# Kernel tuning notes

Hardware: AMD Instinct MI355X
Metric: run time of the kernel (lower is better)

The kernel has to match this reference:

```python
import jax, jax.numpy as jnp
import numpy as np

B, N, K, T = 64, 32768, 128, 512
TMAX = 512  # number of discrete time bins (round(t*10) range)


def setup_inputs() -> dict:
    key = jax.random.key(0)
    k1, k2, k3, k4, k5, k6 = jax.random.split(key, 6)
    state = jax.random.normal(k1, (B, N, 4), dtype=jnp.float32)
    time_idx = jax.random.randint(k2, (B, N), 0, TMAX, dtype=jnp.int32)
    # unique_ids in [-1, K-1]; -1 marks clutter (invalid) measurements
    unique_ids = jax.random.randint(k3, (B, N), 0, K + 1, dtype=jnp.int32) - 1
    # trajectory states [B,K,T,5]: cols [x, y, vx, vy, t] with round(t*10) in 0..TMAX-1
    xy = jax.random.normal(k4, (B, K, T, 2), dtype=jnp.float32)
    vel = jax.random.normal(k5, (B, K, T, 2), dtype=jnp.float32)
    # per-(b,k) permutation of 0..T-1 -> unique times within each trajectory
    times = jnp.argsort(jax.random.uniform(k6, (B, K, T)), axis=-1).astype(jnp.float32)
    traj_states = jnp.concatenate([xy, vel, (times / 10.0)[..., None]], axis=-1)
    return {"state": state, "time_idx": time_idx, "unique_ids": unique_ids,
            "traj_states": traj_states}


def reference(state, time_idx, unique_ids, traj_states):
    xy = state[..., :2]                                   # [B,N,2]
    tvals = jnp.round(traj_states[..., 4] * 10.0).astype(jnp.int32)  # [B,K,T]
    traj_xy = traj_states[..., :2]                        # [B,K,T,2]
    # dense lookup table [B,K,TMAX,2]; default 0 matches torch.zeros_like(tgt)
    b_ix = jnp.arange(B)[:, None, None]
    k_ix = jnp.arange(K)[None, :, None]
    table = jnp.zeros((B, K, TMAX, 2), dtype=state.dtype)
    table = table.at[b_ix, k_ix, tvals].set(traj_xy, mode="drop")
    # gather tgt per measurement by (object id, time bin)
    obj = jnp.clip(unique_ids, 0, K - 1)
    tcl = jnp.clip(time_idx, 0, TMAX - 1)
    tgt = table[jnp.arange(B)[:, None], obj, tcl]         # [B,N,2]
    valid = unique_ids >= 0
    tgt = jnp.where(valid[..., None], tgt, 0.0)
    diff = jnp.abs(xy - tgt).sum(-1)                      # [B,N]
    vf = valid.astype(state.dtype)
    loss = (diff * vf).sum() / vf.sum()
    return loss
```

## Files before the change

kernel.cpp:

```cpp
#include <hip/hip_runtime.h>
#include <hip/hip_fp16.h>

constexpr int Bc = 64;
constexpr int Nc = 32768;
constexpr int Kc = 128;
constexpr int Tc = 512;
constexpr int TMAXc = 512;
constexpr int BK = Bc * Kc;

typedef float f32x4 __attribute__((ext_vector_type(4)));

constexpr size_t TABLE_BYTES = (size_t)Bc * Kc * TMAXc * 4;
constexpr int NBLK2 = 1024;

__global__ __launch_bounds__(256) void build_table_k(
    const f32x4* __restrict__ traj4,
    uint2* __restrict__ table2)
{
    __shared__ __align__(16) float    stage[Tc * 5];
    __shared__ __align__(8)  unsigned tbl[TMAXc];

    const int j   = blockIdx.x;
    const int xcd = j & 7;
    const int s   = j >> 3;
    const int b   = ((s >> 7) << 3) | xcd;
    const int k   = s & 127;
    const int bk  = (b << 7) | k;

    const f32x4* src = traj4 + (size_t)bk * 640;
    for (int t = threadIdx.x; t < 640; t += 256) {
        ((f32x4*)stage)[t] = __builtin_nontemporal_load(&src[t]);
    }
    __syncthreads();

    #pragma unroll
    for (int r = 0; r < 2; ++r) {
        int t = threadIdx.x + r * 256;
        float x  = stage[t * 5 + 0];
        float y  = stage[t * 5 + 1];
        float tv = stage[t * 5 + 4];
        int tau = __float2int_rn(tv * 10.0f);
        if ((unsigned)tau < (unsigned)TMAXc) {
            __half2 p = __floats2half2_rn(x, y);
            unsigned raw;
            __builtin_memcpy(&raw, &p, 4);
            tbl[tau] = raw;
        }
    }
    __syncthreads();

    table2[(size_t)bk * 256 + threadIdx.x] = ((const uint2*)tbl)[threadIdx.x];
}

__global__ __launch_bounds__(256) void gather_reduce_k(
    const f32x4*    __restrict__ state,
    const int*      __restrict__ tidx,
    const int*      __restrict__ uid,
    const unsigned* __restrict__ table,
    float2*         __restrict__ partials)
{
    const int j     = blockIdx.x;
    const int xcd   = j & 7;
    const int s     = j >> 3;
    const int b     = ((s >> 4) << 3) | xcd;
    const int chunk = s & 15;
    const int base  = (b << 15) + (chunk << 11);
    const unsigned* tb = table + ((long long)b << 16);

    f32x4    sv[8];
    int      idv[8], tiv[8];
    unsigned tg[8];

    #pragma unroll
    for (int r = 0; r < 8; ++r) {
        int i = base + r * 256 + threadIdx.x;
        sv[r]  = __builtin_nontemporal_load(&state[i]);
        idv[r] = __builtin_nontemporal_load(&uid[i]);
        tiv[r] = __builtin_nontemporal_load(&tidx[i]);
    }
    #pragma unroll
    for (int r = 0; r < 8; ++r) {
        int obj = min(max(idv[r], 0), Kc - 1);
        int tcl = min(max(tiv[r], 0), TMAXc - 1);
        tg[r] = tb[(obj << 9) + tcl];
    }
    float sum = 0.0f, cnt = 0.0f;
    #pragma unroll
    for (int r = 0; r < 8; ++r) {
        __half2 p;
        __builtin_memcpy(&p, &tg[r], 4);
        float tx = __low2float(p);
        float ty = __high2float(p);
        if (idv[r] >= 0) {
            sum += fabsf(sv[r].x - tx) + fabsf(sv[r].y - ty);
            cnt += 1.0f;
        }
    }

    #pragma unroll
    for (int off = 32; off > 0; off >>= 1) {
        sum += __shfl_down(sum, off, 64);
        cnt += __shfl_down(cnt, off, 64);
    }
    __shared__ float2 lds[4];
    int lane = threadIdx.x & 63;
    int w    = threadIdx.x >> 6;
    if (lane == 0) lds[w] = make_float2(sum, cnt);
    __syncthreads();
    if (threadIdx.x == 0) {
        float s2 = 0.0f, c2 = 0.0f;
        #pragma unroll
        for (int q = 0; q < 4; ++q) { s2 += lds[q].x; c2 += lds[q].y; }
        partials[j] = make_float2(s2, c2);
    }
}

__global__ __launch_bounds__(1024) void final_reduce_k(
    const float2* __restrict__ partials, float* __restrict__ out)
{
    float s, c;
    {
        float2 p = partials[threadIdx.x];
        s = p.x; c = p.y;
    }
    #pragma unroll
    for (int off = 32; off > 0; off >>= 1) {
        s += __shfl_down(s, off, 64);
        c += __shfl_down(c, off, 64);
    }
    __shared__ float2 lds[16];
    int lane = threadIdx.x & 63;
    int w    = threadIdx.x >> 6;
    if (lane == 0) lds[w] = make_float2(s, c);
    __syncthreads();
    if (threadIdx.x == 0) {
        float s2 = 0.0f, c2 = 0.0f;
        #pragma unroll
        for (int q = 0; q < 16; ++q) { s2 += lds[q].x; c2 += lds[q].y; }
        out[0] = s2 / c2;
    }
}

extern "C" void kernel_launch(void* const* d_in, const int* in_sizes, int n_in,
                              void* d_out, int out_size, void* d_ws, size_t ws_size,
                              hipStream_t stream) {
    const f32x4* state = (const f32x4*)d_in[0];
    const int*   tidx  = (const int*)  d_in[1];
    const int*   uid   = (const int*)  d_in[2];
    const f32x4* traj4 = (const f32x4*)d_in[3];
    float* out = (float*)d_out;

    unsigned* table    = (unsigned*)d_ws;
    float2*   partials = (float2*)((char*)d_ws + TABLE_BYTES);

    build_table_k  <<<BK, 256, 0, stream>>>(traj4, (uint2*)table);
    gather_reduce_k<<<NBLK2, 256, 0, stream>>>(state, tidx, uid, table, partials);
    final_reduce_k <<<1, 1024, 0, stream>>>(partials, out);
}
```

Measured before the change: 40.14 us.

## Process two trajectories per block, halve gather blocks, load only xy state

The table-build kernel now handles two (b,k) trajectories per block, with fully unrolled staging loads and two table rows written per block. The gather kernel loads only the x,y half of each state row as an 8-byte vector instead of the full 16-byte row, and each block handles twice as many measurements with half as many blocks. The final reduce shrinks to match. The goal is to cut state read traffic and per-block launch and sync overhead, at the cost of more registers and fewer blocks in flight to hide gather latency.

After: 38.91 us. 1.03x faster.

```diff
diff --git a/kernel.cpp b/kernel.cpp
--- a/kernel.cpp
+++ b/kernel.cpp
@@ -9,32 +9,36 @@
 constexpr int BK = Bc * Kc;
 
 typedef float f32x4 __attribute__((ext_vector_type(4)));
+typedef float f32x2 __attribute__((ext_vector_type(2)));
 
 constexpr size_t TABLE_BYTES = (size_t)Bc * Kc * TMAXc * 4;
-constexpr int NBLK2 = 1024;
+constexpr int NBLK1 = BK / 2;
+constexpr int NBLK2 = 512;
 
 __global__ __launch_bounds__(256) void build_table_k(
     const f32x4* __restrict__ traj4,
     uint2* __restrict__ table2)
 {
-    __shared__ __align__(16) float    stage[Tc * 5];
-    __shared__ __align__(8)  unsigned tbl[TMAXc];
+    __shared__ __align__(16) float    stage[2 * Tc * 5];
+    __shared__ __align__(8)  unsigned tbl[2 * TMAXc];
 
     const int j   = blockIdx.x;
     const int xcd = j & 7;
     const int s   = j >> 3;
-    const int b   = ((s >> 7) << 3) | xcd;
-    const int k   = s & 127;
-    const int bk  = (b << 7) | k;
+    const int b   = ((s >> 6) << 3) | xcd;
+    const int k2  = s & 63;
+    const int bk0 = (b << 7) | (k2 << 1);
 
-    const f32x4* src = traj4 + (size_t)bk * 640;
-    for (int t = threadIdx.x; t < 640; t += 256) {
+    const f32x4* src = traj4 + (size_t)bk0 * 640;
+    #pragma unroll
+    for (int r = 0; r < 5; ++r) {
+        int t = threadIdx.x + r * 256;
         ((f32x4*)stage)[t] = __builtin_nontemporal_load(&src[t]);
     }
     __syncthreads();
 
     #pragma unroll
-    for (int r = 0; r < 2; ++r) {
+    for (int r = 0; r < 4; ++r) {
         int t = threadIdx.x + r * 256;
         float x  = stage[t * 5 + 0];
         float y  = stage[t * 5 + 1];
@@ -44,16 +48,21 @@
             __half2 p = __floats2half2_rn(x, y);
             unsigned raw;
             __builtin_memcpy(&raw, &p, 4);
-            tbl[tau] = raw;
+            tbl[((t >> 9) << 9) + tau] = raw;
         }
     }
     __syncthreads();
 
-    table2[(size_t)bk * 256 + threadIdx.x] = ((const uint2*)tbl)[threadIdx.x];
+    uint2* dst = table2 + (size_t)bk0 * 256;
+    #pragma unroll
+    for (int r = 0; r < 2; ++r) {
+        int t = threadIdx.x + r * 256;
+        dst[t] = ((const uint2*)tbl)[t];
+    }
 }
 
 __global__ __launch_bounds__(256) void gather_reduce_k(
-    const f32x4*    __restrict__ state,
+    const f32x2*    __restrict__ state2,
     const int*      __restrict__ tidx,
     const int*      __restrict__ uid,
     const unsigned* __restrict__ table,
@@ -62,31 +71,31 @@
     const int j     = blockIdx.x;
     const int xcd   = j & 7;
     const int s     = j >> 3;
-    const int b     = ((s >> 4) << 3) | xcd;
-    const int chunk = s & 15;
-    const int base  = (b << 15) + (chunk << 11);
+    const int b     = ((s >> 3) << 3) | xcd;
+    const int chunk = s & 7;
+    const int base  = (b << 15) + (chunk << 12);
     const unsigned* tb = table + ((long long)b << 16);
 
-    f32x4    sv[8];
-    int      idv[8], tiv[8];
-    unsigned tg[8];
+    f32x2    sv[16];
+    int      idv[16], tiv[16];
+    unsigned tg[16];
 
     #pragma unroll
-    for (int r = 0; r < 8; ++r) {
+    for (int r = 0; r < 16; ++r) {
         int i = base + r * 256 + threadIdx.x;
-        sv[r]  = __builtin_nontemporal_load(&state[i]);
+        sv[r]  = __builtin_nontemporal_load(&state2[2 * (size_t)i]);
         idv[r] = __builtin_nontemporal_load(&uid[i]);
         tiv[r] = __builtin_nontemporal_load(&tidx[i]);
     }
     #pragma unroll
-    for (int r = 0; r < 8; ++r) {
+    for (int r = 0; r < 16; ++r) {
         int obj = min(max(idv[r], 0), Kc - 1);
         int tcl = min(max(tiv[r], 0), TMAXc - 1);
         tg[r] = tb[(obj << 9) + tcl];
     }
     float sum = 0.0f, cnt = 0.0f;
     #pragma unroll
-    for (int r = 0; r < 8; ++r) {
+    for (int r = 0; r < 16; ++r) {
         __half2 p;
         __builtin_memcpy(&p, &tg[r], 4);
         float tx = __low2float(p);
@@ -115,7 +124,7 @@
     }
 }
 
-__global__ __launch_bounds__(1024) void final_reduce_k(
+__global__ __launch_bounds__(512) void final_reduce_k(
     const float2* __restrict__ partials, float* __restrict__ out)
 {
     float s, c;
@@ -128,7 +137,7 @@
         s += __shfl_down(s, off, 64);
         c += __shfl_down(c, off, 64);
     }
-    __shared__ float2 lds[16];
+    __shared__ float2 lds[8];
     int lane = threadIdx.x & 63;
     int w    = threadIdx.x >> 6;
     if (lane == 0) lds[w] = make_float2(s, c);
@@ -136,7 +145,7 @@
     if (threadIdx.x == 0) {
         float s2 = 0.0f, c2 = 0.0f;
         #pragma unroll
-        for (int q = 0; q < 16; ++q) { s2 += lds[q].x; c2 += lds[q].y; }
+        for (int q = 0; q < 8; ++q) { s2 += lds[q].x; c2 += lds[q].y; }
         out[0] = s2 / c2;
     }
 }
@@ -144,16 +153,16 @@
 extern "C" void kernel_launch(void* const* d_in, const int* in_sizes, int n_in,
                               void* d_out, int out_size, void* d_ws, size_t ws_size,
                               hipStream_t stream) {
-    const f32x4* state = (const f32x4*)d_in[0];
-    const int*   tidx  = (const int*)  d_in[1];
-    const int*   uid   = (const int*)  d_in[2];
-    const f32x4* traj4 = (const f32x4*)d_in[3];
+    const f32x2* state2 = (const f32x2*)d_in[0];
+    const int*   tidx   = (const int*)  d_in[1];
+    const int*   uid    = (const int*)  d_in[2];
+    const f32x4* traj4  = (const f32x4*)d_in[3];
     float* out = (float*)d_out;
 
     unsigned* table    = (unsigned*)d_ws;
     float2*   partials = (float2*)((char*)d_ws + TABLE_BYTES);
 
-    build_table_k  <<<BK, 256, 0, stream>>>(traj4, (uint2*)table);
-    gather_reduce_k<<<NBLK2, 256, 0, stream>>>(state, tidx, uid, table, partials);
-    final_reduce_k <<<1, 1024, 0, stream>>>(partials, out);
+    build_table_k  <<<NBLK1, 256, 0, stream>>>(traj4, (uint2*)table);
+    gather_reduce_k<<<NBLK2, 256, 0, stream>>>(state2, tidx, uid, table, partials);
+    final_reduce_k <<<1, 512, 0, stream>>>(partials, out);
 }
```
